# Kernel tuning notes

Measured on AMD Instinct MI355X. Metric: run time of the kernel, lower is better.

Reference implementation:

```python
import jax, jax.numpy as jnp
import numpy as np

N_KERNELS = 11

def _kernel_mus(n):
    l = [1.0]
    if n == 1:
        return l
    b = 2.0 / (n - 1)
    l.append(1 - b / 2)
    for i in range(1, n - 1):
        l.append(l[i] - b)
    return l

def _kernel_sigmas(n):
    b = 2.0 / (n - 1)
    l = [0.0001]
    if n == 1:
        return l
    l += [0.5 * b] * (n - 1)
    return l

MU = jnp.asarray(np.array(_kernel_mus(N_KERNELS), dtype=np.float32))      # [K]
SIGMA = jnp.asarray(np.array(_kernel_sigmas(N_KERNELS), dtype=np.float32))  # [K]


def setup_inputs() -> dict:
    key = jax.random.key(0)
    k1, k2, k3, k4 = jax.random.split(key, 4)
    B, Q, D, V, E = 256, 32, 512, 100000, 300
    return {
        "query_tokens": jax.random.randint(k1, (B, Q), 0, V),
        "doc_tokens": jax.random.randint(k2, (B, D), 0, V),
        "emb": jax.random.normal(k3, (V, E), dtype=jnp.float32),
        "fc_w": jax.random.normal(k4, (1, N_KERNELS), dtype=jnp.float32),
        "fc_b": jnp.zeros((1,), dtype=jnp.float32),
    }


def reference(query_tokens, doc_tokens, emb, fc_w, fc_b):
    q_mask = (query_tokens > 0).astype(jnp.float32)  # [B,Q]
    d_mask = (doc_tokens > 0).astype(jnp.float32)    # [B,D]

    qe = emb[query_tokens]  # [B,Q,E]
    de = emb[doc_tokens]    # [B,D,E]

    # Cosine match matrix (CosineMatrixAttention: L2-normalize with tiny eps)
    qn = qe / (jnp.linalg.norm(qe, axis=-1, keepdims=True) + 1e-13)
    dn = de / (jnp.linalg.norm(de, axis=-1, keepdims=True) + 1e-13)
    mm = jnp.einsum("bqe,bde->bqd", qn, dn)  # [B,Q,D]

    mask = q_mask[:, :, None] * d_mask[:, None, :]  # [B,Q,D]
    mm = mm * mask

    # Gaussian RBF kernel pooling: [B,Q,D,K]
    diff = mm[..., None] - MU[None, None, None, :]
    rbf = jnp.exp(-jnp.square(diff) / (2.0 * jnp.square(SIGMA)[None, None, None, :]))
    rbf = rbf * mask[..., None]

    query_kernels = rbf.sum(axis=2)  # [B,Q,K]
    log_qk = jnp.log(jnp.maximum(query_kernels, 1e-10)) * 0.01
    # NOTE: original code computes a masked version but (bug) sums the UNMASKED
    # log_query_kernels; we faithfully replicate that.
    kernels = log_qk.sum(axis=1)  # [B,K]

    score = kernels @ fc_w.T + fc_b  # [B,1]
    return score
```

## Files before the change

### kernel.cpp

```cpp
#include <hip/hip_runtime.h>
#include <hip/hip_bf16.h>
#include <math.h>


#define NB 256
#define NQ 32
#define ND 512
#define NE 300
#define NF4 75
#define LROW 328
#define SPLITS 2
#define DPB 256
#define CHUNK 64
#define NCHUNK 4
#define NT 512
#define NK 11
#define QK_SZ (NQ * NK)

typedef __bf16 bf16x8 __attribute__((ext_vector_type(8)));
typedef __bf16 bf16x4 __attribute__((ext_vector_type(4)));
typedef float f32x4 __attribute__((ext_vector_type(4)));

__global__ __launch_bounds__(NT, 4) void knrm_main(
    const int* __restrict__ qtok,
    const int* __restrict__ dtok,
    const float* __restrict__ emb,
    float* __restrict__ partial)
{
  __shared__ __align__(16) __bf16 qlds[NQ][LROW];
  __shared__ __align__(16) __bf16 dlds[CHUNK][LROW];
  __shared__ float qscale[NQ];
  __shared__ float dscale[CHUNK];
  __shared__ float qkl[QK_SZ];

  const int b    = blockIdx.x >> 1;
  const int sp   = blockIdx.x & 1;
  const int t    = threadIdx.x;
  const int lane = t & 63;
  const int w    = t >> 6;

  if (t < QK_SZ && (t % NK) != 0) qkl[t] = 0.0f;

  {
    const int r = t >> 4;
    const int j = t & 15;
    const int tq = qtok[b * NQ + r];
    const float4* rowp = (const float4*)(emb + (size_t)tq * NE);

    float4 v[5];
    #pragma unroll
    for (int i = 0; i < 4; ++i) v[i] = rowp[j + 16 * i];
    v[4] = (j < 11) ? rowp[j + 64] : make_float4(0.f, 0.f, 0.f, 0.f);

    float ss = 0.0f;
    #pragma unroll
    for (int i = 0; i < 5; ++i) {
      ss += v[i].x * v[i].x + v[i].y * v[i].y + v[i].z * v[i].z + v[i].w * v[i].w;
      if (i < 4 || j < 11) {
        bf16x4 h;
        h[0] = (__bf16)v[i].x; h[1] = (__bf16)v[i].y;
        h[2] = (__bf16)v[i].z; h[3] = (__bf16)v[i].w;
        *(bf16x4*)&qlds[r][4 * (j + 16 * i)] = h;
      }
    }
    if (j < 5) {
      bf16x4 z = {};
      *(bf16x4*)&qlds[r][NE + 4 * j] = z;
    }
    ss += __shfl_xor(ss, 1, 16);
    ss += __shfl_xor(ss, 2, 16);
    ss += __shfl_xor(ss, 4, 16);
    ss += __shfl_xor(ss, 8, 16);
    if (j == 0) qscale[r] = (tq > 0) ? 1.0f / (sqrtf(ss) + 1e-13f) : 0.0f;

    int cnt = 0;
    #pragma unroll
    for (int jj = 0; jj < DPB / 16; ++jj) {
      int td = dtok[b * ND + sp * DPB + j + 16 * jj];
      cnt += (tq > 0 && td == tq) ? 1 : 0;
    }
    cnt += __shfl_xor(cnt, 1, 16);
    cnt += __shfl_xor(cnt, 2, 16);
    cnt += __shfl_xor(cnt, 4, 16);
    cnt += __shfl_xor(cnt, 8, 16);
    if (j == 0) qkl[r * NK] = (float)cnt;
  }

  const int mt  = w >> 2;
  const int nt  = w & 3;
  const int l15 = lane & 15;
  const int l4  = lane >> 4;

  float rbfacc[4][10];
  #pragma unroll
  for (int r4 = 0; r4 < 4; ++r4)
    #pragma unroll
    for (int k = 0; k < 10; ++k) rbfacc[r4][k] = 0.0f;

  const __bf16* aptr = &qlds[mt * 16 + l15][l4 * 8];
  const __bf16* bptr = &dlds[nt * 16 + l15][l4 * 8];

  const float muk[10] = {0.9f, 0.7f, 0.5f, 0.3f, 0.1f,
                         -0.1f, -0.3f, -0.5f, -0.7f, -0.9f};

  #pragma unroll 1
  for (int ch = 0; ch < NCHUNK; ++ch) {
    __syncthreads();
    {
      const int r = t >> 3;
      const int j = t & 7;
      const int td = dtok[b * ND + sp * DPB + ch * CHUNK + r];
      const float4* rowp = (const float4*)(emb + (size_t)td * NE);

      float4 v[10];
      #pragma unroll
      for (int i = 0; i < 9; ++i) v[i] = rowp[j + 8 * i];
      v[9] = (j < 3) ? rowp[j + 72] : make_float4(0.f, 0.f, 0.f, 0.f);

      float ss = 0.0f;
      #pragma unroll
      for (int i = 0; i < 10; ++i) {
        ss += v[i].x * v[i].x + v[i].y * v[i].y + v[i].z * v[i].z + v[i].w * v[i].w;
        if (i < 9 || j < 3) {
          bf16x4 h;
          h[0] = (__bf16)v[i].x; h[1] = (__bf16)v[i].y;
          h[2] = (__bf16)v[i].z; h[3] = (__bf16)v[i].w;
          *(bf16x4*)&dlds[r][4 * (j + 8 * i)] = h;
        }
      }
      if (j < 5) {
        bf16x4 z = {};
        *(bf16x4*)&dlds[r][NE + 4 * j] = z;
      }
      ss += __shfl_xor(ss, 1, 8);
      ss += __shfl_xor(ss, 2, 8);
      ss += __shfl_xor(ss, 4, 8);
      if (j == 0) dscale[r] = (td > 0) ? 1.0f / (sqrtf(ss) + 1e-13f) : 0.0f;
    }
    __syncthreads();

    f32x4 acc = {};
    #pragma unroll
    for (int k = 0; k < 10; ++k) {
      bf16x8 av = *(const bf16x8*)(aptr + k * 32);
      bf16x8 bv = *(const bf16x8*)(bptr + k * 32);
      acc = __builtin_amdgcn_mfma_f32_16x16x32_bf16(av, bv, acc, 0, 0, 0);
    }

    const float ds = dscale[nt * 16 + l15];
    #pragma unroll
    for (int r4 = 0; r4 < 4; ++r4) {
      const float qs = qscale[mt * 16 + l4 * 4 + r4];
      const float s = qs * ds;
      const float mm = (s == 0.0f) ? 1e8f : acc[r4] * s;
      #pragma unroll
      for (int k = 0; k < 10; ++k) {
        float d = mm - muk[k];
        rbfacc[r4][k] += __builtin_amdgcn_exp2f(d * d * -72.13475204444817f);
      }
    }
  }

  #pragma unroll
  for (int r4 = 0; r4 < 4; ++r4)
    #pragma unroll
    for (int k = 0; k < 10; ++k) {
      float v = rbfacc[r4][k];
      v += __shfl_xor(v, 1);
      v += __shfl_xor(v, 2);
      v += __shfl_xor(v, 4);
      v += __shfl_xor(v, 8);
      if (l15 == 0) atomicAdd(&qkl[(mt * 16 + l4 * 4 + r4) * NK + k + 1], v);
    }
  __syncthreads();

  float* pp = partial + ((size_t)b * SPLITS + sp) * QK_SZ;
  for (int i = t; i < QK_SZ; i += NT) pp[i] = qkl[i];
}

__global__ __launch_bounds__(64) void knrm_epi(
    const float* __restrict__ partial,
    const float* __restrict__ fcw,
    const float* __restrict__ fcb,
    float* __restrict__ out)
{
  const int b = blockIdx.x;
  const int lane = threadIdx.x;
  const float* pb = partial + (size_t)b * SPLITS * QK_SZ;
  float acc = 0.0f;
  for (int i = lane; i < QK_SZ; i += 64) {
    float s = pb[i] + pb[i + QK_SZ];
    int k = i % NK;
    acc += logf(fmaxf(s, 1e-10f)) * 0.01f * fcw[k];
  }
  #pragma unroll
  for (int off = 1; off < 64; off <<= 1) acc += __shfl_xor(acc, off);
  if (lane == 0) out[b] = acc + fcb[0];
}

extern "C" void kernel_launch(void* const* d_in, const int* in_sizes, int n_in,
                              void* d_out, int out_size, void* d_ws, size_t ws_size,
                              hipStream_t stream) {
  const int* qtok = (const int*)d_in[0];
  const int* dtok = (const int*)d_in[1];
  const float* emb = (const float*)d_in[2];
  const float* fcw = (const float*)d_in[3];
  const float* fcb = (const float*)d_in[4];
  float* out = (float*)d_out;
  float* partial = (float*)d_ws;

  knrm_main<<<NB * SPLITS, NT, 0, stream>>>(qtok, dtok, emb, partial);
  knrm_epi<<<NB, 64, 0, stream>>>(partial, fcw, fcb, out);
}
```

Baseline: 196.8 us.

## Prefetch next doc chunk into registers and fuse epilogue via last-block counter

Doc embedding rows for the next chunk are now loaded from global memory into registers while the MFMA and RBF work runs on the current chunk, so gather latency overlaps compute. The q-scale loads are hoisted out of the chunk loop. The separate epilogue kernel is replaced by an atomic completion counter, so the second split block for each batch finishes the log-sum and FC step itself. In exchange this adds a memset launch, an extra barrier per chunk, higher register pressure from the prefetch buffer, and one wasted prefetch on the last iteration.

```diff
diff --git a/kernel.cpp b/kernel.cpp
--- a/kernel.cpp
+++ b/kernel.cpp
@@ -16,6 +16,7 @@
 #define NT 512
 #define NK 11
 #define QK_SZ (NQ * NK)
+#define PART_BYTES (NB * SPLITS * QK_SZ * 4)
 
 typedef __bf16 bf16x8 __attribute__((ext_vector_type(8)));
 typedef __bf16 bf16x4 __attribute__((ext_vector_type(4)));
@@ -25,13 +26,18 @@
     const int* __restrict__ qtok,
     const int* __restrict__ dtok,
     const float* __restrict__ emb,
-    float* __restrict__ partial)
+    const float* __restrict__ fcw,
+    const float* __restrict__ fcb,
+    float* __restrict__ partial,
+    int* __restrict__ done_cnt,
+    float* __restrict__ out)
 {
   __shared__ __align__(16) __bf16 qlds[NQ][LROW];
   __shared__ __align__(16) __bf16 dlds[CHUNK][LROW];
   __shared__ float qscale[NQ];
   __shared__ float dscale[CHUNK];
   __shared__ float qkl[QK_SZ];
+  __shared__ int last_flag;
 
   const int b    = blockIdx.x >> 1;
   const int sp   = blockIdx.x & 1;
@@ -39,6 +45,21 @@
   const int lane = t & 63;
   const int w    = t >> 6;
 
+  const int dr = t >> 3;
+  const int dj = t & 7;
+  int td4[NCHUNK];
+  #pragma unroll
+  for (int ch = 0; ch < NCHUNK; ++ch)
+    td4[ch] = dtok[b * ND + sp * DPB + ch * CHUNK + dr];
+
+  float4 v[10];
+  {
+    const float4* rowp = (const float4*)(emb + (size_t)td4[0] * NE);
+    #pragma unroll
+    for (int i = 0; i < 9; ++i) v[i] = rowp[dj + 8 * i];
+    v[9] = (dj < 3) ? rowp[dj + 72] : make_float4(0.f, 0.f, 0.f, 0.f);
+  }
+
   if (t < QK_SZ && (t % NK) != 0) qkl[t] = 0.0f;
 
   {
@@ -47,26 +68,23 @@
     const int tq = qtok[b * NQ + r];
     const float4* rowp = (const float4*)(emb + (size_t)tq * NE);
 
-    float4 v[5];
-    #pragma unroll
-    for (int i = 0; i < 4; ++i) v[i] = rowp[j + 16 * i];
-    v[4] = (j < 11) ? rowp[j + 64] : make_float4(0.f, 0.f, 0.f, 0.f);
+    float4 qv[5];
+    #pragma unroll
+    for (int i = 0; i < 4; ++i) qv[i] = rowp[j + 16 * i];
+    qv[4] = (j < 11) ? rowp[j + 64] : make_float4(0.f, 0.f, 0.f, 0.f);
 
     float ss = 0.0f;
     #pragma unroll
     for (int i = 0; i < 5; ++i) {
-      ss += v[i].x * v[i].x + v[i].y * v[i].y + v[i].z * v[i].z + v[i].w * v[i].w;
+      ss += qv[i].x * qv[i].x + qv[i].y * qv[i].y + qv[i].z * qv[i].z + qv[i].w * qv[i].w;
       if (i < 4 || j < 11) {
         bf16x4 h;
-        h[0] = (__bf16)v[i].x; h[1] = (__bf16)v[i].y;
-        h[2] = (__bf16)v[i].z; h[3] = (__bf16)v[i].w;
+        h[0] = (__bf16)qv[i].x; h[1] = (__bf16)qv[i].y;
+        h[2] = (__bf16)qv[i].z; h[3] = (__bf16)qv[i].w;
         *(bf16x4*)&qlds[r][4 * (j + 16 * i)] = h;
       }
     }
-    if (j < 5) {
-      bf16x4 z = {};
-      *(bf16x4*)&qlds[r][NE + 4 * j] = z;
-    }
+    if (j < 5) { bf16x4 z = {}; *(bf16x4*)&qlds[r][NE + 4 * j] = z; }
     ss += __shfl_xor(ss, 1, 16);
     ss += __shfl_xor(ss, 2, 16);
     ss += __shfl_xor(ss, 4, 16);
@@ -85,6 +103,7 @@
     cnt += __shfl_xor(cnt, 8, 16);
     if (j == 0) qkl[r * NK] = (float)cnt;
   }
+  __syncthreads();
 
   const int mt  = w >> 2;
   const int nt  = w & 3;
@@ -100,44 +119,42 @@
   const __bf16* aptr = &qlds[mt * 16 + l15][l4 * 8];
   const __bf16* bptr = &dlds[nt * 16 + l15][l4 * 8];
 
+  float qs[4];
+  #pragma unroll
+  for (int r4 = 0; r4 < 4; ++r4) qs[r4] = qscale[mt * 16 + l4 * 4 + r4];
+
   const float muk[10] = {0.9f, 0.7f, 0.5f, 0.3f, 0.1f,
                          -0.1f, -0.3f, -0.5f, -0.7f, -0.9f};
 
   #pragma unroll 1
   for (int ch = 0; ch < NCHUNK; ++ch) {
-    __syncthreads();
     {
-      const int r = t >> 3;
-      const int j = t & 7;
-      const int td = dtok[b * ND + sp * DPB + ch * CHUNK + r];
-      const float4* rowp = (const float4*)(emb + (size_t)td * NE);
-
-      float4 v[10];
-      #pragma unroll
-      for (int i = 0; i < 9; ++i) v[i] = rowp[j + 8 * i];
-      v[9] = (j < 3) ? rowp[j + 72] : make_float4(0.f, 0.f, 0.f, 0.f);
-
       float ss = 0.0f;
       #pragma unroll
       for (int i = 0; i < 10; ++i) {
         ss += v[i].x * v[i].x + v[i].y * v[i].y + v[i].z * v[i].z + v[i].w * v[i].w;
-        if (i < 9 || j < 3) {
+        if (i < 9 || dj < 3) {
           bf16x4 h;
           h[0] = (__bf16)v[i].x; h[1] = (__bf16)v[i].y;
           h[2] = (__bf16)v[i].z; h[3] = (__bf16)v[i].w;
-          *(bf16x4*)&dlds[r][4 * (j + 8 * i)] = h;
+          *(bf16x4*)&dlds[dr][4 * (dj + 8 * i)] = h;
         }
       }
-      if (j < 5) {
-        bf16x4 z = {};
-        *(bf16x4*)&dlds[r][NE + 4 * j] = z;
-      }
+      if (dj < 5) { bf16x4 z = {}; *(bf16x4*)&dlds[dr][NE + 4 * dj] = z; }
       ss += __shfl_xor(ss, 1, 8);
       ss += __shfl_xor(ss, 2, 8);
       ss += __shfl_xor(ss, 4, 8);
-      if (j == 0) dscale[r] = (td > 0) ? 1.0f / (sqrtf(ss) + 1e-13f) : 0.0f;
+      if (dj == 0) dscale[dr] = (td4[ch] > 0) ? 1.0f / (sqrtf(ss) + 1e-13f) : 0.0f;
     }
     __syncthreads();
+
+    {
+      const int chn = (ch + 1) & (NCHUNK - 1);
+      const float4* rowp = (const float4*)(emb + (size_t)td4[chn] * NE);
+      #pragma unroll
+      for (int i = 0; i < 9; ++i) v[i] = rowp[dj + 8 * i];
+      v[9] = (dj < 3) ? rowp[dj + 72] : make_float4(0.f, 0.f, 0.f, 0.f);
+    }
 
     f32x4 acc = {};
     #pragma unroll
@@ -150,8 +167,7 @@
     const float ds = dscale[nt * 16 + l15];
     #pragma unroll
     for (int r4 = 0; r4 < 4; ++r4) {
-      const float qs = qscale[mt * 16 + l4 * 4 + r4];
-      const float s = qs * ds;
+      const float s = qs[r4] * ds;
       const float mm = (s == 0.0f) ? 1e8f : acc[r4] * s;
       #pragma unroll
       for (int k = 0; k < 10; ++k) {
@@ -159,43 +175,44 @@
         rbfacc[r4][k] += __builtin_amdgcn_exp2f(d * d * -72.13475204444817f);
       }
     }
+    __syncthreads();
   }
 
   #pragma unroll
   for (int r4 = 0; r4 < 4; ++r4)
     #pragma unroll
     for (int k = 0; k < 10; ++k) {
-      float v = rbfacc[r4][k];
-      v += __shfl_xor(v, 1);
-      v += __shfl_xor(v, 2);
-      v += __shfl_xor(v, 4);
-      v += __shfl_xor(v, 8);
-      if (l15 == 0) atomicAdd(&qkl[(mt * 16 + l4 * 4 + r4) * NK + k + 1], v);
+      float vv = rbfacc[r4][k];
+      vv += __shfl_xor(vv, 1);
+      vv += __shfl_xor(vv, 2);
+      vv += __shfl_xor(vv, 4);
+      vv += __shfl_xor(vv, 8);
+      if (l15 == 0) atomicAdd(&qkl[(mt * 16 + l4 * 4 + r4) * NK + k + 1], vv);
     }
   __syncthreads();
 
   float* pp = partial + ((size_t)b * SPLITS + sp) * QK_SZ;
   for (int i = t; i < QK_SZ; i += NT) pp[i] = qkl[i];
-}
-
-__global__ __launch_bounds__(64) void knrm_epi(
-    const float* __restrict__ partial,
-    const float* __restrict__ fcw,
-    const float* __restrict__ fcb,
-    float* __restrict__ out)
-{
-  const int b = blockIdx.x;
-  const int lane = threadIdx.x;
-  const float* pb = partial + (size_t)b * SPLITS * QK_SZ;
-  float acc = 0.0f;
-  for (int i = lane; i < QK_SZ; i += 64) {
-    float s = pb[i] + pb[i + QK_SZ];
-    int k = i % NK;
-    acc += logf(fmaxf(s, 1e-10f)) * 0.01f * fcw[k];
-  }
-  #pragma unroll
-  for (int off = 1; off < 64; off <<= 1) acc += __shfl_xor(acc, off);
-  if (lane == 0) out[b] = acc + fcb[0];
+  __syncthreads();
+
+  if (t == 0) {
+    __threadfence();
+    int old = atomicAdd(&done_cnt[b], 1);
+    last_flag = (old == 1);
+  }
+  __syncthreads();
+  if (last_flag && w == 0) {
+    __threadfence();
+    const float* po = partial + ((size_t)b * SPLITS + (sp ^ 1)) * QK_SZ;
+    float acc = 0.0f;
+    for (int i = lane; i < QK_SZ; i += 64) {
+      float s = qkl[i] + po[i];
+      acc += logf(fmaxf(s, 1e-10f)) * 0.01f * fcw[i % NK];
+    }
+    #pragma unroll
+    for (int off = 1; off < 64; off <<= 1) acc += __shfl_xor(acc, off);
+    if (lane == 0) out[b] = acc + fcb[0];
+  }
 }
 
 extern "C" void kernel_launch(void* const* d_in, const int* in_sizes, int n_in,
@@ -208,7 +225,9 @@
   const float* fcb = (const float*)d_in[4];
   float* out = (float*)d_out;
   float* partial = (float*)d_ws;
-
-  knrm_main<<<NB * SPLITS, NT, 0, stream>>>(qtok, dtok, emb, partial);
-  knrm_epi<<<NB, 64, 0, stream>>>(partial, fcw, fcb, out);
+  int* done_cnt = (int*)((char*)d_ws + PART_BYTES);
+
+  hipMemsetAsync(done_cnt, 0, NB * sizeof(int), stream);
+  knrm_main<<<NB * SPLITS, NT, 0, stream>>>(qtok, dtok, emb, fcw, fcb,
+                                            partial, done_cnt, out);
 }
```

Result: slower. 216.8 us (+10.2%).

## Warp-specialize main kernel into producer and consumer waves with double-buffered doc tiles

Applied to the files above, without the earlier changes.

Splits the 8 waves into 4 producer waves that gather, normalize and bf16-convert the next 32-row document chunk into a second LDS buffer, and 4 consumer waves that run MFMA and RBF pooling on the current chunk. The aim is to overlap the global embedding gather with compute instead of serializing load then compute per chunk. In exchange only half the waves do math, so each consumer wave handles twice the tiles, and the chunk count doubles, which adds barriers.

```diff
diff --git a/kernel.cpp b/kernel.cpp
--- a/kernel.cpp
+++ b/kernel.cpp
@@ -7,12 +7,11 @@
 #define NQ 32
 #define ND 512
 #define NE 300
-#define NF4 75
 #define LROW 328
 #define SPLITS 2
 #define DPB 256
-#define CHUNK 64
-#define NCHUNK 4
+#define CHUNK 32
+#define NCHUNK 8
 #define NT 512
 #define NK 11
 #define QK_SZ (NQ * NK)
@@ -28,9 +27,9 @@
     float* __restrict__ partial)
 {
   __shared__ __align__(16) __bf16 qlds[NQ][LROW];
-  __shared__ __align__(16) __bf16 dlds[CHUNK][LROW];
+  __shared__ __align__(16) __bf16 dlds[2][CHUNK][LROW];
   __shared__ float qscale[NQ];
-  __shared__ float dscale[CHUNK];
+  __shared__ float dscale[2][CHUNK];
   __shared__ float qkl[QK_SZ];
 
   const int b    = blockIdx.x >> 1;
@@ -38,140 +37,143 @@
   const int t    = threadIdx.x;
   const int lane = t & 63;
   const int w    = t >> 6;
-
-  if (t < QK_SZ && (t % NK) != 0) qkl[t] = 0.0f;
-
-  {
-    const int r = t >> 4;
-    const int j = t & 15;
-    const int tq = qtok[b * NQ + r];
-    const float4* rowp = (const float4*)(emb + (size_t)tq * NE);
-
-    float4 v[5];
-    #pragma unroll
-    for (int i = 0; i < 4; ++i) v[i] = rowp[j + 16 * i];
-    v[4] = (j < 11) ? rowp[j + 64] : make_float4(0.f, 0.f, 0.f, 0.f);
+  const bool producer = (w < 4);
+
+  auto stage = [&](int ch, int buf) {
+    const int dr = t >> 3;
+    const int dj = t & 7;
+    const int td = dtok[b * ND + sp * DPB + ch * CHUNK + dr];
+    const float4* rowp = (const float4*)(emb + (size_t)td * NE);
+
+    float4 v[10];
+    #pragma unroll
+    for (int i = 0; i < 9; ++i) v[i] = rowp[dj + 8 * i];
+    v[9] = (dj < 3) ? rowp[dj + 72] : make_float4(0.f, 0.f, 0.f, 0.f);
 
     float ss = 0.0f;
     #pragma unroll
-    for (int i = 0; i < 5; ++i) {
+    for (int i = 0; i < 10; ++i) {
       ss += v[i].x * v[i].x + v[i].y * v[i].y + v[i].z * v[i].z + v[i].w * v[i].w;
-      if (i < 4 || j < 11) {
+      if (i < 9 || dj < 3) {
         bf16x4 h;
         h[0] = (__bf16)v[i].x; h[1] = (__bf16)v[i].y;
         h[2] = (__bf16)v[i].z; h[3] = (__bf16)v[i].w;
-        *(bf16x4*)&qlds[r][4 * (j + 16 * i)] = h;
-      }
-    }
-    if (j < 5) {
-      bf16x4 z = {};
-      *(bf16x4*)&qlds[r][NE + 4 * j] = z;
-    }
-    ss += __shfl_xor(ss, 1, 16);
-    ss += __shfl_xor(ss, 2, 16);
-    ss += __shfl_xor(ss, 4, 16);
-    ss += __shfl_xor(ss, 8, 16);
+        *(bf16x4*)&dlds[buf][dr][4 * (dj + 8 * i)] = h;
+      }
+    }
+    if (dj < 5) { bf16x4 z = {}; *(bf16x4*)&dlds[buf][dr][NE + 4 * dj] = z; }
+    ss += __shfl_xor(ss, 1, 8);
+    ss += __shfl_xor(ss, 2, 8);
+    ss += __shfl_xor(ss, 4, 8);
+    if (dj == 0) dscale[buf][dr] = (td > 0) ? 1.0f / (sqrtf(ss) + 1e-13f) : 0.0f;
+  };
+
+  if (producer) {
+    for (int i = t; i < QK_SZ; i += 256)
+      if (i % NK) qkl[i] = 0.0f;
+    stage(0, 0);
+  } else {
+    const int r = (t >> 3) & 31;
+    const int j = t & 7;
+    const int tq = qtok[b * NQ + r];
+    const float4* rowp = (const float4*)(emb + (size_t)tq * NE);
+
+    float4 qv[10];
+    #pragma unroll
+    for (int i = 0; i < 9; ++i) qv[i] = rowp[j + 8 * i];
+    qv[9] = (j < 3) ? rowp[j + 72] : make_float4(0.f, 0.f, 0.f, 0.f);
+
+    float ss = 0.0f;
+    #pragma unroll
+    for (int i = 0; i < 10; ++i) {
+      ss += qv[i].x * qv[i].x + qv[i].y * qv[i].y + qv[i].z * qv[i].z + qv[i].w * qv[i].w;
+      if (i < 9 || j < 3) {
+        bf16x4 h;
+        h[0] = (__bf16)qv[i].x; h[1] = (__bf16)qv[i].y;
+        h[2] = (__bf16)qv[i].z; h[3] = (__bf16)qv[i].w;
+        *(bf16x4*)&qlds[r][4 * (j + 8 * i)] = h;
+      }
+    }
+    if (j < 5) { bf16x4 z = {}; *(bf16x4*)&qlds[r][NE + 4 * j] = z; }
+    ss += __shfl_xor(ss, 1, 8);
+    ss += __shfl_xor(ss, 2, 8);
+    ss += __shfl_xor(ss, 4, 8);
     if (j == 0) qscale[r] = (tq > 0) ? 1.0f / (sqrtf(ss) + 1e-13f) : 0.0f;
 
     int cnt = 0;
-    #pragma unroll
-    for (int jj = 0; jj < DPB / 16; ++jj) {
-      int td = dtok[b * ND + sp * DPB + j + 16 * jj];
+    #pragma unroll 4
+    for (int jj = 0; jj < 32; ++jj) {
+      int td = dtok[b * ND + sp * DPB + j + 8 * jj];
       cnt += (tq > 0 && td == tq) ? 1 : 0;
     }
-    cnt += __shfl_xor(cnt, 1, 16);
-    cnt += __shfl_xor(cnt, 2, 16);
-    cnt += __shfl_xor(cnt, 4, 16);
-    cnt += __shfl_xor(cnt, 8, 16);
+    cnt += __shfl_xor(cnt, 1, 8);
+    cnt += __shfl_xor(cnt, 2, 8);
+    cnt += __shfl_xor(cnt, 4, 8);
     if (j == 0) qkl[r * NK] = (float)cnt;
   }
-
-  const int mt  = w >> 2;
-  const int nt  = w & 3;
-  const int l15 = lane & 15;
-  const int l4  = lane >> 4;
-
+  __syncthreads();
+
+  const int cw   = w - 4;
+  const int mt   = cw >> 1;
+  const int nt   = cw & 1;
+  const int l15  = lane & 15;
+  const int quad = lane >> 4;
+
+  const float muk[10] = {0.9f, 0.7f, 0.5f, 0.3f, 0.1f,
+                         -0.1f, -0.3f, -0.5f, -0.7f, -0.9f};
   float rbfacc[4][10];
   #pragma unroll
   for (int r4 = 0; r4 < 4; ++r4)
     #pragma unroll
     for (int k = 0; k < 10; ++k) rbfacc[r4][k] = 0.0f;
 
-  const __bf16* aptr = &qlds[mt * 16 + l15][l4 * 8];
-  const __bf16* bptr = &dlds[nt * 16 + l15][l4 * 8];
-
-  const float muk[10] = {0.9f, 0.7f, 0.5f, 0.3f, 0.1f,
-                         -0.1f, -0.3f, -0.5f, -0.7f, -0.9f};
+  const __bf16* aptr = &qlds[((mt < 0 ? 0 : mt) * 16 + l15) & 31][quad * 8];
 
   #pragma unroll 1
   for (int ch = 0; ch < NCHUNK; ++ch) {
+    if (producer) {
+      if (ch + 1 < NCHUNK) stage(ch + 1, (ch + 1) & 1);
+    } else {
+      const int buf = ch & 1;
+      const __bf16* bptr = &dlds[buf][nt * 16 + l15][quad * 8];
+
+      f32x4 acc = {};
+      #pragma unroll
+      for (int kk = 0; kk < 10; ++kk) {
+        bf16x8 av = *(const bf16x8*)(aptr + kk * 32);
+        bf16x8 bv = *(const bf16x8*)(bptr + kk * 32);
+        acc = __builtin_amdgcn_mfma_f32_16x16x32_bf16(av, bv, acc, 0, 0, 0);
+      }
+
+      const float ds = dscale[buf][nt * 16 + l15];
+      #pragma unroll
+      for (int r4 = 0; r4 < 4; ++r4) {
+        const float qs = qscale[mt * 16 + quad * 4 + r4];
+        const float s = qs * ds;
+        const float mm = (s == 0.0f) ? 1e8f : acc[r4] * s;
+        #pragma unroll
+        for (int k = 0; k < 10; ++k) {
+          float d = mm - muk[k];
+          rbfacc[r4][k] += __builtin_amdgcn_exp2f(d * d * -72.13475204444817f);
+        }
+      }
+    }
     __syncthreads();
-    {
-      const int r = t >> 3;
-      const int j = t & 7;
-      const int td = dtok[b * ND + sp * DPB + ch * CHUNK + r];
-      const float4* rowp = (const float4*)(emb + (size_t)td * NE);
-
-      float4 v[10];
-      #pragma unroll
-      for (int i = 0; i < 9; ++i) v[i] = rowp[j + 8 * i];
-      v[9] = (j < 3) ? rowp[j + 72] : make_float4(0.f, 0.f, 0.f, 0.f);
-
-      float ss = 0.0f;
-      #pragma unroll
-      for (int i = 0; i < 10; ++i) {
-        ss += v[i].x * v[i].x + v[i].y * v[i].y + v[i].z * v[i].z + v[i].w * v[i].w;
-        if (i < 9 || j < 3) {
-          bf16x4 h;
-          h[0] = (__bf16)v[i].x; h[1] = (__bf16)v[i].y;
-          h[2] = (__bf16)v[i].z; h[3] = (__bf16)v[i].w;
-          *(bf16x4*)&dlds[r][4 * (j + 8 * i)] = h;
-        }
-      }
-      if (j < 5) {
-        bf16x4 z = {};
-        *(bf16x4*)&dlds[r][NE + 4 * j] = z;
-      }
-      ss += __shfl_xor(ss, 1, 8);
-      ss += __shfl_xor(ss, 2, 8);
-      ss += __shfl_xor(ss, 4, 8);
-      if (j == 0) dscale[r] = (td > 0) ? 1.0f / (sqrtf(ss) + 1e-13f) : 0.0f;
-    }
-    __syncthreads();
-
-    f32x4 acc = {};
-    #pragma unroll
-    for (int k = 0; k < 10; ++k) {
-      bf16x8 av = *(const bf16x8*)(aptr + k * 32);
-      bf16x8 bv = *(const bf16x8*)(bptr + k * 32);
-      acc = __builtin_amdgcn_mfma_f32_16x16x32_bf16(av, bv, acc, 0, 0, 0);
-    }
-
-    const float ds = dscale[nt * 16 + l15];
-    #pragma unroll
-    for (int r4 = 0; r4 < 4; ++r4) {
-      const float qs = qscale[mt * 16 + l4 * 4 + r4];
-      const float s = qs * ds;
-      const float mm = (s == 0.0f) ? 1e8f : acc[r4] * s;
+  }
+
+  if (!producer) {
+    #pragma unroll
+    for (int r4 = 0; r4 < 4; ++r4)
       #pragma unroll
       for (int k = 0; k < 10; ++k) {
-        float d = mm - muk[k];
-        rbfacc[r4][k] += __builtin_amdgcn_exp2f(d * d * -72.13475204444817f);
-      }
-    }
-  }
-
-  #pragma unroll
-  for (int r4 = 0; r4 < 4; ++r4)
-    #pragma unroll
-    for (int k = 0; k < 10; ++k) {
-      float v = rbfacc[r4][k];
-      v += __shfl_xor(v, 1);
-      v += __shfl_xor(v, 2);
-      v += __shfl_xor(v, 4);
-      v += __shfl_xor(v, 8);
-      if (l15 == 0) atomicAdd(&qkl[(mt * 16 + l4 * 4 + r4) * NK + k + 1], v);
-    }
+        float vv = rbfacc[r4][k];
+        vv += __shfl_xor(vv, 1);
+        vv += __shfl_xor(vv, 2);
+        vv += __shfl_xor(vv, 4);
+        vv += __shfl_xor(vv, 8);
+        if (l15 == 0) atomicAdd(&qkl[(mt * 16 + quad * 4 + r4) * NK + k + 1], vv);
+      }
+  }
   __syncthreads();
 
   float* pp = partial + ((size_t)b * SPLITS + sp) * QK_SZ;
@@ -190,8 +192,7 @@
   float acc = 0.0f;
   for (int i = lane; i < QK_SZ; i += 64) {
     float s = pb[i] + pb[i + QK_SZ];
-    int k = i % NK;
-    acc += logf(fmaxf(s, 1e-10f)) * 0.01f * fcw[k];
+    acc += logf(fmaxf(s, 1e-10f)) * 0.01f * fcw[i % NK];
   }
   #pragma unroll
   for (int off = 1; off < 64; off <<= 1) acc += __shfl_xor(acc, off);
```

Measured after the change: 193.4 us. About the same (-1.7%).
